# Optimization experiments

Hardware: AMD Instinct MI355X
Metric: run time of the kernel (lower is better)

The kernel has to match this reference:

```python
import jax, jax.numpy as jnp
import numpy as np

N_BLOCKS = 2
C = 64
N_HEADS = 4
FF = 256
NB_SEQ = 40
SEQ_LEN = 512
NB_PAIRS = (NB_SEQ * (NB_SEQ - 1)) // 2  # 780
B = 2
EPS_ATT = 1e-6


def _ln(x, g, b, eps=1e-5):
    # LayerNorm over last axis (channels)
    mu = jnp.mean(x, axis=-1, keepdims=True)
    var = jnp.var(x, axis=-1, keepdims=True)
    return (x - mu) * jax.lax.rsqrt(var + eps) * g + b


def _kernel_attn(x, wq, bq, wk, bk, wv, bv, wp, bp):
    # x: [B, M, T, C]; faithful to KernelAxialMultiAttention.
    Bs, M, T, Cc = x.shape
    N, D = N_HEADS, Cc // N_HEADS
    q = jax.nn.elu(x @ wq.T + bq) + 1.0
    k = jax.nn.elu(x @ wk.T + bk) + 1.0
    v = x @ wv.T + bv
    q = q.reshape(Bs, M, T, N, D)
    k = k.reshape(Bs, M, T, N, D)
    v = v.reshape(Bs, M, T, N, D)
    ksum = k.sum(axis=2)                                   # [B,M,N,D]
    z = 1.0 / (jnp.einsum('bmtnd,bmnd->bmtn', q, ksum) + EPS_ATT)  # [B,M,T,N]
    ktv = jnp.einsum('bmtnd,bmtne->bmnde', k, v)           # [B,M,N,D,D]
    # Original does Z.expand(...,T,D) @ KtV where Z's D columns are identical,
    # which equals z * column-sum of KtV (sum over first D axis).
    ktv_cs = ktv.sum(axis=-2)                              # [B,M,N,D]
    V = z[..., None] * ktv_cs[:, :, None, :, :]            # [B,M,T,N,D]
    V = V.reshape(Bs, M, T, Cc)
    return V @ wp.T + bp


def setup_inputs() -> dict:
    key = jax.random.key(0)
    ks = iter(jax.random.split(key, 64))

    def w(shape, scale=0.05):
        return jax.random.normal(next(ks), shape, dtype=jnp.float32) * scale

    # seq2pair gather matrix [P, S]
    ii, jj = np.triu_indices(NB_SEQ, 1)
    sp = np.zeros((NB_PAIRS, NB_SEQ), np.float32)
    sp[np.arange(NB_PAIRS), ii] = 1.0
    sp[np.arange(NB_PAIRS), jj] = 1.0

    inp = {
        'x': jax.random.normal(next(ks), (B, 22, SEQ_LEN, NB_SEQ), dtype=jnp.float32),
        'w_in': w((C, 22)), 'b_in': jnp.zeros((C,), jnp.float32),
        'g0': jnp.ones((C,), jnp.float32), 'be0': jnp.zeros((C,), jnp.float32),
        'rqw': w((N_BLOCKS, C, C)), 'rqb': jnp.zeros((N_BLOCKS, C), jnp.float32),
        'rkw': w((N_BLOCKS, C, C)), 'rkb': jnp.zeros((N_BLOCKS, C), jnp.float32),
        'rvw': w((N_BLOCKS, C, C)), 'rvb': jnp.zeros((N_BLOCKS, C), jnp.float32),
        'rpw': w((N_BLOCKS, C, C)), 'rpb': jnp.zeros((N_BLOCKS, C), jnp.float32),
        'cqw': w((N_BLOCKS, C, C)), 'cqb': jnp.zeros((N_BLOCKS, C), jnp.float32),
        'ckw': w((N_BLOCKS, C, C)), 'ckb': jnp.zeros((N_BLOCKS, C), jnp.float32),
        'cvw': w((N_BLOCKS, C, C)), 'cvb': jnp.zeros((N_BLOCKS, C), jnp.float32),
        'cpw': w((N_BLOCKS, C, C)), 'cpb': jnp.zeros((N_BLOCKS, C), jnp.float32),
        'ln_g': jnp.ones((N_BLOCKS, C), jnp.float32), 'ln_b': jnp.zeros((N_BLOCKS, C), jnp.float32),
        'f1w': w((N_BLOCKS, FF, C)), 'f1b': jnp.zeros((N_BLOCKS, FF), jnp.float32),
        'f2w': w((N_BLOCKS, C, FF)), 'f2b': jnp.zeros((N_BLOCKS, C), jnp.float32),
        'wout': w((1, C)), 'bout': jnp.zeros((1,), jnp.float32),
        'seq2pair': jnp.asarray(sp),
    }
    return inp


def reference(x, w_in, b_in, g0, be0, rqw, rqb, rkw, rkb, rvw, rvb, rpw, rpb,
              cqw, cqb, ckw, ckb, cvw, cvb, cpw, cpb, ln_g, ln_b,
              f1w, f1b, f2w, f2b, wout, bout, seq2pair):
    # block_1_1: 1x1 conv (22->64) + ReLU; x: [B,22,L,S] -> h: [B,C,L,S]
    h = jax.nn.relu(jnp.einsum('bcls,dc->bdls', x, w_in) + b_in[None, :, None, None])
    # seq2pair gather-sum: [B,P,L,C] channel-last representation
    hp = jnp.einsum('ps,bdls->bpld', seq2pair, h)
    hp = _ln(hp, g0, be0)
    for i in range(N_BLOCKS):
        # row attention over seq_len axis (M=P, T=L)
        att = _kernel_attn(hp, rqw[i], rqb[i], rkw[i], rkb[i], rvw[i], rvb[i], rpw[i], rpb[i])
        hp = att + hp
        hp = _ln(hp, ln_g[i], ln_b[i])
        # column attention over pairs axis (M=L, T=P)
        hc = jnp.swapaxes(hp, 1, 2)  # [B,L,P,C]
        att = _kernel_attn(hc, cqw[i], cqb[i], ckw[i], ckb[i], cvw[i], cvb[i], cpw[i], cpb[i])
        hp = jnp.swapaxes(att, 1, 2) + hp
        hp = _ln(hp, ln_g[i], ln_b[i])
        # FFN: 1x1 conv 64->256 GELU 256->64, residual
        f = jax.nn.gelu(hp @ f1w[i].T + f1b[i], approximate=False)
        hp = (f @ f2w[i].T + f2b[i]) + hp
        if i != N_BLOCKS - 1:
            hp = _ln(hp, ln_g[i], ln_b[i])
    # pwFNN: 1x1 conv 64->1 + Softplus, then mean over seq_len axis
    y = jax.nn.softplus(hp @ wout.T + bout)[..., 0]   # [B,P,L]
    return jnp.mean(y, axis=-1)                        # [B,P]
```

## Files before the change

### kernel.cpp

```cpp
#include <hip/hip_runtime.h>
#include <math.h>
#include <stdint.h>

#define B_   2
#define S_   40
#define P_   780
#define L_   512
#define C_   64
#define FF_  256
#define NTOK (B_*P_*L_)

typedef __attribute__((ext_vector_type(8))) short short8;
typedef __attribute__((ext_vector_type(4))) float f32x4;
typedef __attribute__((ext_vector_type(4))) unsigned int u32x4;

__device__ __forceinline__ float ln64(float r, float g, float b) {
    float s1 = r, s2 = r * r;
    #pragma unroll
    for (int m = 1; m < 64; m <<= 1) {
        s1 += __shfl_xor(s1, m, 64);
        s2 += __shfl_xor(s2, m, 64);
    }
    float mu  = s1 * (1.0f / 64.0f);
    float var = s2 * (1.0f / 64.0f) - mu * mu;
    return (r - mu) * rsqrtf(var + 1e-5f) * g + b;
}

__device__ __forceinline__ float gelu_fast(float x) {
    float x2 = x * x;
    float u  = x * fmaf(0.044715f, x2, 1.0f);
    float e  = __builtin_amdgcn_exp2f(u * 2.302265106f);
    return x * e * __builtin_amdgcn_rcpf(e + 1.0f);
}
__device__ __forceinline__ float softplus_f(float v) {
    return (v > 20.0f) ? v : log1pf(__expf(v));
}
__device__ __forceinline__ float elup1(float v) {
    return (v > 0.0f) ? v + 1.0f : __expf(v);
}
__device__ __forceinline__ unsigned short f2bf(float f) {
    union { float f; uint32_t u; } cv; cv.f = f;
    uint32_t u = cv.u;
    return (unsigned short)((u + 0x7FFFu + ((u >> 16) & 1u)) >> 16);
}
__device__ __forceinline__ short8 pack8(f32x4 a, f32x4 b) {
    short8 v;
    v[0]=(short)f2bf(a[0]); v[1]=(short)f2bf(a[1]); v[2]=(short)f2bf(a[2]); v[3]=(short)f2bf(a[3]);
    v[4]=(short)f2bf(b[0]); v[5]=(short)f2bf(b[1]); v[6]=(short)f2bf(b[2]); v[7]=(short)f2bf(b[3]);
    return v;
}
__device__ __forceinline__ uint32_t cvtpk(float a, float b) {
    uint32_t d;
    asm("v_cvt_pk_bf16_f32 %0, %1, %2" : "=v"(d) : "v"(a), "v"(b));
    return d;
}

__global__ void k_conv_in(const float* __restrict__ x, const float* __restrict__ w_in,
                          const float* __restrict__ b_in, float* __restrict__ h) {
    int gid = blockIdx.x * 256 + threadIdx.x;
    int c  = gid & 63;
    int tk = gid >> 6;
    if (tk >= B_ * L_ * S_) return;
    int b = tk / (L_ * S_);
    int r = tk % (L_ * S_);
    int l = r / S_;
    int s = r % S_;
    float acc = b_in[c];
    const float* xb = x + (size_t)b * 22 * L_ * S_ + (size_t)l * S_ + s;
    #pragma unroll
    for (int cc = 0; cc < 22; cc++)
        acc = fmaf(xb[(size_t)cc * L_ * S_], w_in[c * 22 + cc], acc);
    h[gid] = fmaxf(acc, 0.0f);
}

__global__ void k_gather_ln(const float* __restrict__ h, const float* __restrict__ g0,
                            const float* __restrict__ be0, float* __restrict__ hp) {
    int lane = threadIdx.x & 63;
    int wv   = threadIdx.x >> 6;
    int tk = blockIdx.x * 4 + wv;
    if (tk >= NTOK) return;
    int b = tk / (P_ * L_);
    int r = tk % (P_ * L_);
    int p = r / L_;
    int l = r % L_;
    int i = 0, rem = p, cnt = S_ - 1;
    while (rem >= cnt) { rem -= cnt; cnt--; i++; }
    int j = i + 1 + rem;
    const float* hb = h + (((size_t)b * L_ + l) * S_) * 64;
    float v = hb[i * 64 + lane] + hb[j * 64 + lane];
    hp[(size_t)tk * 64 + lane] = ln64(v, g0[lane], be0[lane]);
}

__global__ void k_wprep_qkv(const float* __restrict__ rqw, const float* __restrict__ rkw,
                            const float* __restrict__ rvw, const float* __restrict__ cqw,
                            const float* __restrict__ ckw, const float* __restrict__ cvw,
                            unsigned short* __restrict__ qkvf) {
    int g = blockIdx.x * 256 + threadIdx.x;
    if (g >= 6144) return;
    int m = g >> 9, r = g & 511;
    int mat = m >> 1, layer = m & 1;
    int q = r >> 6, lane = r & 63;
    int c = lane & 15, hi = lane >> 4;
    int nt = q >> 1, s = q & 1;
    const float* base;
    switch (mat) {
        case 0: base = rqw; break; case 1: base = rkw; break; case 2: base = rvw; break;
        case 3: base = cqw; break; case 4: base = ckw; break; default: base = cvw; break;
    }
    const float* src = base + layer * 4096 + (nt * 16 + c) * 64 + s * 32 + hi * 8;
    short8 v;
    #pragma unroll
    for (int i = 0; i < 8; i++) v[i] = (short)f2bf(src[i]);
    *(short8*)(qkvf + (size_t)m * 4096 + (size_t)r * 8) = v;
}

template <bool ROW>
__global__ __launch_bounds__(512) void k_attn_red(
        const float* __restrict__ hp, const unsigned short* __restrict__ wkf,
        const unsigned short* __restrict__ wvf, const float* __restrict__ bk,
        const float* __restrict__ bv, const float* __restrict__ wp,
        float* __restrict__ stats) {
    __shared__ float redK[8][64];
    __shared__ float redV[8][64];
    __shared__ float kvfin[64];

    const int tid = threadIdx.x, lane = tid & 63, w8 = tid >> 6;
    const int t = lane & 15, hi = lane >> 4;
    const int slice = blockIdx.x;
    const int T  = ROW ? L_ : P_;
    const int NT = ROW ? 32 : 49;

    size_t rowbase, rowstep;
    if (ROW) { rowbase = (size_t)slice * L_ * 64; rowstep = 64; }
    else     { int b = slice >> 9, l = slice & 511;
               rowbase = ((size_t)b * P_ * L_ + l) * 64; rowstep = (size_t)L_ * 64; }

    short8 wkfr[4][2], wvfr[4][2];
    #pragma unroll
    for (int nt = 0; nt < 4; nt++)
        #pragma unroll
        for (int s = 0; s < 2; s++) {
            wkfr[nt][s] = *(const short8*)(wkf + ((size_t)((nt*2+s)*64 + lane)) * 8);
            wvfr[nt][s] = *(const short8*)(wvf + ((size_t)((nt*2+s)*64 + lane)) * 8);
        }
    f32x4 bkL[4], bvL[4];
    #pragma unroll
    for (int nt = 0; nt < 4; nt++) {
        bkL[nt] = *(const f32x4*)(bk + nt * 16 + hi * 4);
        bvL[nt] = *(const f32x4*)(bv + nt * 16 + hi * 4);
    }

    float ks[4][4] = {}, kv[4][4] = {};

    for (int tile = w8; tile < NT; tile += 8) {
        int tok = tile * 16 + t;
        bool valid = ROW || (tok < T);
        int tokc = valid ? tok : (T - 1);
        const float* src = hp + rowbase + (size_t)tokc * rowstep;
        short8 xf[2];
        #pragma unroll
        for (int s = 0; s < 2; s++) {
            f32x4 a  = *(const f32x4*)(src + s * 32 + hi * 8);
            f32x4 b2 = *(const f32x4*)(src + s * 32 + hi * 8 + 4);
            xf[s] = pack8(a, b2);
        }
        f32x4 aK[4], aV[4];
        #pragma unroll
        for (int nt = 0; nt < 4; nt++) { aK[nt] = (f32x4){0,0,0,0}; aV[nt] = (f32x4){0,0,0,0}; }
        #pragma unroll
        for (int nt = 0; nt < 4; nt++)
            #pragma unroll
            for (int s = 0; s < 2; s++) {
                aK[nt] = __builtin_amdgcn_mfma_f32_16x16x32_bf16(wkfr[nt][s], xf[s], aK[nt], 0, 0, 0);
                aV[nt] = __builtin_amdgcn_mfma_f32_16x16x32_bf16(wvfr[nt][s], xf[s], aV[nt], 0, 0, 0);
            }
        #pragma unroll
        for (int nt = 0; nt < 4; nt++) {
            float kk[4], vv[4];
            #pragma unroll
            for (int r = 0; r < 4; r++) {
                kk[r] = valid ? elup1(aK[nt][r] + bkL[nt][r]) : 0.0f;
                vv[r] = valid ? (aV[nt][r] + bvL[nt][r]) : 0.0f;
            }
            float sp = kk[0] + kk[1] + kk[2] + kk[3];
            sp += __shfl_xor(sp, 16, 64);
            sp += __shfl_xor(sp, 32, 64);
            #pragma unroll
            for (int r = 0; r < 4; r++) { ks[nt][r] += kk[r]; kv[nt][r] += sp * vv[r]; }
        }
    }

    #pragma unroll
    for (int nt = 0; nt < 4; nt++)
        #pragma unroll
        for (int r = 0; r < 4; r++) {
            #pragma unroll
            for (int m = 1; m < 16; m <<= 1) {
                ks[nt][r] += __shfl_xor(ks[nt][r], m, 64);
                kv[nt][r] += __shfl_xor(kv[nt][r], m, 64);
            }
        }
    if (t == 0) {
        #pragma unroll
        for (int nt = 0; nt < 4; nt++)
            #pragma unroll
            for (int r = 0; r < 4; r++) {
                redK[w8][nt * 16 + hi * 4 + r] = ks[nt][r];
                redV[w8][nt * 16 + hi * 4 + r] = kv[nt][r];
            }
    }
    __syncthreads();
    if (tid < 64) {
        float a = 0.0f, b2 = 0.0f;
        #pragma unroll
        for (int w = 0; w < 8; w++) { a += redK[w][tid]; b2 += redV[w][tid]; }
        stats[(size_t)slice * 320 + tid] = a;
        kvfin[tid] = b2;
    }
    __syncthreads();
    if (tid < 256) {
        int c = tid & 63, n = tid >> 6;
        const float* wpr = wp + c * 64 + n * 16;
        float s = 0.0f;
        #pragma unroll
        for (int e = 0; e < 16; e++) s = fmaf(kvfin[n * 16 + e], wpr[e], s);
        stats[(size_t)slice * 320 + 64 + c * 4 + n] = s;
    }
}

__global__ __launch_bounds__(256) void k_attn_map_row(
        float* __restrict__ hp, const unsigned short* __restrict__ wqf,
        const float* __restrict__ bq, const float* __restrict__ bp,
        const float* __restrict__ stats, const float* __restrict__ lng,
        const float* __restrict__ lnb) {
    const int tid = threadIdx.x, lane = tid & 63, w4 = tid >> 6;
    const int t = lane & 15, hi = lane >> 4;
    const int slice = blockIdx.x >> 3;
    const int tok = ((blockIdx.x & 7) * 4 + w4) * 16 + t;
    const size_t off = ((size_t)slice * L_ + tok) * 64;

    const float* src = hp + off;
    short8 xf[2];
    #pragma unroll
    for (int s = 0; s < 2; s++) {
        f32x4 a  = *(const f32x4*)(src + s * 32 + hi * 8);
        f32x4 b2 = *(const f32x4*)(src + s * 32 + hi * 8 + 4);
        xf[s] = pack8(a, b2);
    }
    f32x4 aQ[4];
    #pragma unroll
    for (int nt = 0; nt < 4; nt++) aQ[nt] = (f32x4){0,0,0,0};
    #pragma unroll
    for (int nt = 0; nt < 4; nt++)
        #pragma unroll
        for (int s = 0; s < 2; s++) {
            short8 wfr = *(const short8*)(wqf + ((size_t)((nt*2+s)*64 + lane)) * 8);
            aQ[nt] = __builtin_amdgcn_mfma_f32_16x16x32_bf16(wfr, xf[s], aQ[nt], 0, 0, 0);
        }

    const float* st = stats + (size_t)slice * 320;
    float z[4];
    #pragma unroll
    for (int nt = 0; nt < 4; nt++) {
        f32x4 bq4 = *(const f32x4*)(bq + nt * 16 + hi * 4);
        f32x4 kS  = *(const f32x4*)(st + nt * 16 + hi * 4);
        float d = 0.0f;
        #pragma unroll
        for (int r = 0; r < 4; r++)
            d = fmaf(elup1(aQ[nt][r] + bq4[r]), kS[r], d);
        d += __shfl_xor(d, 16, 64);
        d += __shfl_xor(d, 32, 64);
        z[nt] = 1.0f / (d + 1e-6f);
    }

    float o[4][4];
    float s1 = 0.0f, s2 = 0.0f;
    #pragma unroll
    for (int nt = 0; nt < 4; nt++) {
        f32x4 bp4 = *(const f32x4*)(bp + nt * 16 + hi * 4);
        f32x4 xr  = *(const f32x4*)(src + nt * 16 + hi * 4);
        #pragma unroll
        for (int r = 0; r < 4; r++) {
            int ch = nt * 16 + hi * 4 + r;
            f32x4 wv4 = *(const f32x4*)(st + 64 + ch * 4);
            float val = z[0] * wv4[0] + z[1] * wv4[1] + z[2] * wv4[2] + z[3] * wv4[3]
                      + bp4[r] + xr[r];
            o[nt][r] = val;
            s1 += val; s2 += val * val;
        }
    }
    s1 += __shfl_xor(s1, 16, 64);  s1 += __shfl_xor(s1, 32, 64);
    s2 += __shfl_xor(s2, 16, 64);  s2 += __shfl_xor(s2, 32, 64);
    float mu  = s1 * (1.0f / 64.0f);
    float var = s2 * (1.0f / 64.0f) - mu * mu;
    float rs  = rsqrtf(var + 1e-5f);
    #pragma unroll
    for (int nt = 0; nt < 4; nt++) {
        f32x4 g4 = *(const f32x4*)(lng + nt * 16 + hi * 4);
        f32x4 b4 = *(const f32x4*)(lnb + nt * 16 + hi * 4);
        f32x4 res;
        #pragma unroll
        for (int r = 0; r < 4; r++)
            res[r] = (o[nt][r] - mu) * rs * g4[r] + b4[r];
        *(f32x4*)(hp + off + nt * 16 + hi * 4) = res;
    }
}

__global__ void k_wprep(const float* __restrict__ f1w, const float* __restrict__ f2w,
                        unsigned short* __restrict__ w1s, unsigned short* __restrict__ w2s) {
    int g = blockIdx.x * 256 + threadIdx.x;
    if (g >= 8192) return;
    int layer = g >> 12;
    int rem   = g & 4095;
    int which = rem >> 11;
    int idx   = rem & 2047;
    int l  = idx & 63;
    int q  = idx >> 6;
    int c  = l & 15, hi = l >> 4;
    const float* src;
    unsigned short* dst;
    if (which == 0) {
        int s = q & 1, nt = q >> 1;
        src = f1w + (size_t)layer * 16384 + (nt * 16 + c) * 64 + s * 32 + hi * 8;
        dst = w1s + (size_t)layer * 16384 + (size_t)idx * 8;
    } else {
        int s = q & 7, nt = q >> 3;
        src = f2w + (size_t)layer * 16384 + (nt * 16 + c) * 256 + s * 32 + hi * 8;
        dst = w2s + (size_t)layer * 16384 + (size_t)idx * 8;
    }
    short8 v;
    #pragma unroll
    for (int i = 0; i < 8; i++) v[i] = (short)f2bf(src[i]);
    *(short8*)dst = v;
}

template <int MODE>
__global__ __launch_bounds__(256) void k_cmap_ffn(
        float* __restrict__ hp, const unsigned short* __restrict__ wqf,
        const float* __restrict__ bq, const float* __restrict__ bpv,
        const float* __restrict__ stats,
        const unsigned short* __restrict__ w1s, const float* __restrict__ f1b,
        const unsigned short* __restrict__ w2s, const float* __restrict__ f2b,
        const float* __restrict__ lng, const float* __restrict__ lnb,
        const float* __restrict__ wout, const float* __restrict__ bout,
        float* __restrict__ out) {
    __shared__ __align__(16) unsigned char Ylds[4][2048];
    __shared__ __align__(16) unsigned char G2[4][8192];

    const int tid = threadIdx.x, lane = tid & 63, wv = tid >> 6;
    const int c = lane & 15, hi = lane >> 4;
    const int slice = blockIdx.x / 13, tile = blockIdx.x % 13;
    const int b = slice >> 9, l = slice & 511;
    const int p = (tile * 4 + wv) * 16 + c;
    const bool valid = p < P_;
    const int pc = valid ? p : P_ - 1;
    const size_t off = (((size_t)b * P_ + pc) * L_ + l) * 64;
    const float* src = hp + off;

    short8 xf[2];
    #pragma unroll
    for (int s = 0; s < 2; s++) {
        f32x4 a  = *(const f32x4*)(src + s * 32 + hi * 8);
        f32x4 b2 = *(const f32x4*)(src + s * 32 + hi * 8 + 4);
        xf[s] = pack8(a, b2);
    }
    f32x4 aQ[4];
    #pragma unroll
    for (int nt = 0; nt < 4; nt++) aQ[nt] = (f32x4){0,0,0,0};
    #pragma unroll
    for (int nt = 0; nt < 4; nt++)
        #pragma unroll
        for (int s = 0; s < 2; s++) {
            short8 wfr = *(const short8*)(wqf + ((size_t)((nt*2+s)*64 + lane)) * 8);
            aQ[nt] = __builtin_amdgcn_mfma_f32_16x16x32_bf16(wfr, xf[s], aQ[nt], 0, 0, 0);
        }
    const float* st = stats + (size_t)slice * 320;
    float z[4];
    #pragma unroll
    for (int nt = 0; nt < 4; nt++) {
        f32x4 bq4 = *(const f32x4*)(bq + nt * 16 + hi * 4);
        f32x4 kS  = *(const f32x4*)(st + nt * 16 + hi * 4);
        float d = 0.0f;
        #pragma unroll
        for (int r = 0; r < 4; r++)
            d = fmaf(elup1(aQ[nt][r] + bq4[r]), kS[r], d);
        d += __shfl_xor(d, 16, 64);
        d += __shfl_xor(d, 32, 64);
        z[nt] = 1.0f / (d + 1e-6f);
    }

    float vv[4][4];
    {
        float s1 = 0.0f, s2 = 0.0f;
        #pragma unroll
        for (int nt = 0; nt < 4; nt++) {
            f32x4 bp4 = *(const f32x4*)(bpv + nt * 16 + hi * 4);
            f32x4 xr  = *(const f32x4*)(src + nt * 16 + hi * 4);
            #pragma unroll
            for (int r = 0; r < 4; r++) {
                int ch = nt * 16 + hi * 4 + r;
                f32x4 wv4 = *(const f32x4*)(st + 64 + ch * 4);
                float val = z[0] * wv4[0] + z[1] * wv4[1] + z[2] * wv4[2] + z[3] * wv4[3]
                          + bp4[r] + xr[r];
                vv[nt][r] = val;
                s1 += val; s2 += val * val;
            }
        }
        s1 += __shfl_xor(s1, 16, 64);  s1 += __shfl_xor(s1, 32, 64);
        s2 += __shfl_xor(s2, 16, 64);  s2 += __shfl_xor(s2, 32, 64);
        float mu  = s1 * (1.0f / 64.0f);
        float var = s2 * (1.0f / 64.0f) - mu * mu;
        float rs  = rsqrtf(var + 1e-5f);
        #pragma unroll
        for (int nt = 0; nt < 4; nt++) {
            f32x4 g4 = *(const f32x4*)(lng + nt * 16 + hi * 4);
            f32x4 b4 = *(const f32x4*)(lnb + nt * 16 + hi * 4);
            #pragma unroll
            for (int r = 0; r < 4; r++)
                vv[nt][r] = (vv[nt][r] - mu) * rs * g4[r] + b4[r];
        }
    }

    unsigned char* yw = &Ylds[wv][0];
    #pragma unroll
    for (int nt = 0; nt < 4; nt++) {
        uint2 w = make_uint2(cvtpk(vv[nt][0], vv[nt][1]), cvtpk(vv[nt][2], vv[nt][3]));
        uint32_t ch0 = nt * 16 + hi * 4;
        uint32_t boff = (uint32_t)c * 128 + ((ch0 >> 3) ^ (uint32_t)(c & 7)) * 16 + (ch0 & 7) * 2;
        *(uint2*)(yw + boff) = w;
    }
    short8 xb2[2];
    #pragma unroll
    for (int s = 0; s < 2; s++)
        xb2[s] = *(short8*)(yw + (uint32_t)c * 128 +
                            (((uint32_t)(s * 4 + hi)) ^ (uint32_t)(c & 7)) * 16);

    unsigned char* g2w = &G2[wv][0] + c * 512;
    #pragma unroll
    for (int nt = 0; nt < 16; nt++) {
        f32x4 acc = *(const f32x4*)(f1b + nt * 16 + hi * 4);
        #pragma unroll
        for (int s = 0; s < 2; s++) {
            short8 wf = *(const short8*)(w1s + ((size_t)(nt * 2 + s) * 64 + lane) * 8);
            acc = __builtin_amdgcn_mfma_f32_16x16x32_bf16(wf, xb2[s], acc, 0, 0, 0);
        }
        uint32_t p0 = cvtpk(gelu_fast(acc[0]), gelu_fast(acc[1]));
        uint32_t p1 = cvtpk(gelu_fast(acc[2]), gelu_fast(acc[3]));
        uint32_t woff = ((uint32_t)(nt * 32 + hi * 8)) ^ ((uint32_t)c << 4);
        *(uint2*)(g2w + woff) = make_uint2(p0, p1);
    }

    f32x4 acc2[4];
    #pragma unroll
    for (int n2 = 0; n2 < 4; n2++)
        acc2[n2] = *(const f32x4*)(f2b + n2 * 16 + hi * 4);
    #pragma unroll
    for (int s = 0; s < 8; s++) {
        uint32_t roff = ((uint32_t)(s * 64 + hi * 16)) ^ ((uint32_t)c << 4);
        short8 fa = *(short8*)(g2w + roff);
        #pragma unroll
        for (int n2 = 0; n2 < 4; n2++) {
            short8 wf = *(const short8*)(w2s + ((size_t)(n2 * 8 + s) * 64 + lane) * 8);
            acc2[n2] = __builtin_amdgcn_mfma_f32_16x16x32_bf16(wf, fa, acc2[n2], 0, 0, 0);
        }
    }

    float vo[4][4];
    float s1 = 0.0f, s2 = 0.0f;
    #pragma unroll
    for (int n2 = 0; n2 < 4; n2++)
        #pragma unroll
        for (int r = 0; r < 4; r++) {
            float v = acc2[n2][r] + vv[n2][r];
            vo[n2][r] = v;
            s1 += v; s2 += v * v;
        }

    if (MODE == 0) {
        s1 += __shfl_xor(s1, 16, 64);  s1 += __shfl_xor(s1, 32, 64);
        s2 += __shfl_xor(s2, 16, 64);  s2 += __shfl_xor(s2, 32, 64);
        float mu  = s1 * (1.0f / 64.0f);
        float var = s2 * (1.0f / 64.0f) - mu * mu;
        float rs  = rsqrtf(var + 1e-5f);
        if (valid) {
            float* drow = hp + off;
            #pragma unroll
            for (int n2 = 0; n2 < 4; n2++) {
                f32x4 g4 = *(const f32x4*)(lng + n2 * 16 + hi * 4);
                f32x4 b4 = *(const f32x4*)(lnb + n2 * 16 + hi * 4);
                f32x4 res;
                #pragma unroll
                for (int r = 0; r < 4; r++)
                    res[r] = (vo[n2][r] - mu) * rs * g4[r] + b4[r];
                *(f32x4*)(drow + n2 * 16 + hi * 4) = res;
            }
        }
    } else {
        float part = 0.0f;
        #pragma unroll
        for (int n2 = 0; n2 < 4; n2++) {
            f32x4 w4 = *(const f32x4*)(wout + n2 * 16 + hi * 4);
            #pragma unroll
            for (int r = 0; r < 4; r++)
                part = fmaf(vo[n2][r], w4[r], part);
        }
        part += __shfl_xor(part, 16, 64);
        part += __shfl_xor(part, 32, 64);
        if (hi == 0 && valid) {
            float sp = softplus_f(part + bout[0]);
            atomicAdd(out + b * P_ + pc, sp * (1.0f / L_));
        }
    }
}

extern "C" void kernel_launch(void* const* d_in, const int* in_sizes, int n_in,
                              void* d_out, int out_size, void* d_ws, size_t ws_size,
                              hipStream_t stream) {
    const float* x    = (const float*)d_in[0];
    const float* w_in = (const float*)d_in[1];
    const float* b_in = (const float*)d_in[2];
    const float* g0   = (const float*)d_in[3];
    const float* be0  = (const float*)d_in[4];
    const float* rqw  = (const float*)d_in[5];  const float* rqb = (const float*)d_in[6];
    const float* rkw  = (const float*)d_in[7];  const float* rkb = (const float*)d_in[8];
    const float* rvw  = (const float*)d_in[9];  const float* rvb = (const float*)d_in[10];
    const float* rpw  = (const float*)d_in[11]; const float* rpb = (const float*)d_in[12];
    const float* cqw  = (const float*)d_in[13]; const float* cqb = (const float*)d_in[14];
    const float* ckw  = (const float*)d_in[15]; const float* ckb = (const float*)d_in[16];
    const float* cvw  = (const float*)d_in[17]; const float* cvb = (const float*)d_in[18];
    const float* cpw  = (const float*)d_in[19]; const float* cpb = (const float*)d_in[20];
    const float* lng  = (const float*)d_in[21]; const float* lnb = (const float*)d_in[22];
    const float* f1w  = (const float*)d_in[23]; const float* f1b = (const float*)d_in[24];
    const float* f2w  = (const float*)d_in[25]; const float* f2b = (const float*)d_in[26];
    const float* wout = (const float*)d_in[27]; const float* bout= (const float*)d_in[28];
    float* out = (float*)d_out;

    float* hp = (float*)d_ws;
    float* h  = hp + (size_t)NTOK * 64;
    unsigned short* w1s  = (unsigned short*)h;
    unsigned short* w2s  = w1s + 2 * 16384;
    unsigned short* qkvf = w2s + 2 * 16384;
    float* stats = (float*)(qkvf + 12 * 4096);

    hipMemsetAsync(out, 0, (size_t)out_size * sizeof(float), stream);

    k_conv_in<<<(B_ * L_ * S_ * 64) / 256, 256, 0, stream>>>(x, w_in, b_in, h);
    k_gather_ln<<<NTOK / 4, 256, 0, stream>>>(h, g0, be0, hp);
    k_wprep<<<32, 256, 0, stream>>>(f1w, f2w, w1s, w2s);
    k_wprep_qkv<<<24, 256, 0, stream>>>(rqw, rkw, rvw, cqw, ckw, cvw, qkvf);

    for (int i = 0; i < 2; i++) {
        k_attn_red<true><<<B_ * P_, 512, 0, stream>>>(hp,
            qkvf + (size_t)(2 + i) * 4096, qkvf + (size_t)(4 + i) * 4096,
            rkb + i * 64, rvb + i * 64, rpw + i * 4096, stats);
        k_attn_map_row<<<B_ * P_ * 8, 256, 0, stream>>>(hp,
            qkvf + (size_t)(0 + i) * 4096, rqb + i * 64, rpb + i * 64,
            stats, lng + i * 64, lnb + i * 64);
        k_attn_red<false><<<B_ * L_, 512, 0, stream>>>(hp,
            qkvf + (size_t)(8 + i) * 4096, qkvf + (size_t)(10 + i) * 4096,
            ckb + i * 64, cvb + i * 64, cpw + i * 4096, stats);
        if (i == 0) {
            k_cmap_ffn<0><<<B_ * L_ * 13, 256, 0, stream>>>(hp,
                qkvf + (size_t)(6 + i) * 4096, cqb + i * 64, cpb + i * 64, stats,
                w1s + (size_t)i * 16384, f1b + i * 256,
                w2s + (size_t)i * 16384, f2b + i * 64,
                lng + i * 64, lnb + i * 64, wout, bout, out);
        } else {
            k_cmap_ffn<1><<<B_ * L_ * 13, 256, 0, stream>>>(hp,
                qkvf + (size_t)(6 + i) * 4096, cqb + i * 64, cpb + i * 64, stats,
                w1s + (size_t)i * 16384, f1b + i * 256,
                w2s + (size_t)i * 16384, f2b + i * 64,
                lng + i * 64, lnb + i * 64, wout, bout, out);
        }
    }
}
```

Measured before the change: 1.171 ms.

## Store activations as bf16 with transposed copy for column attention

The activation buffer moves from fp32 to bf16 storage. The row-attention map kernel now writes a second, transposed [B,L,P,C] copy, so column-attention kernels read contiguous rows instead of doing strided gathers. The FFN GELU staging in LDS is split into two halves, which halves shared memory per block and may raise occupancy. This cuts global traffic and conversion work, but the residual stream now loses precision on every stage because it is rounded to bf16.

New measurement: 1.175 ms. Within noise of the previous version (+0.3%).

```diff
diff --git a/kernel.cpp b/kernel.cpp
--- a/kernel.cpp
+++ b/kernel.cpp
@@ -12,7 +12,7 @@
 
 typedef __attribute__((ext_vector_type(8))) short short8;
 typedef __attribute__((ext_vector_type(4))) float f32x4;
-typedef __attribute__((ext_vector_type(4))) unsigned int u32x4;
+typedef __attribute__((ext_vector_type(4))) unsigned short us4;
 
 __device__ __forceinline__ float ln64(float r, float g, float b) {
     float s1 = r, s2 = r * r;
@@ -25,7 +25,6 @@
     float var = s2 * (1.0f / 64.0f) - mu * mu;
     return (r - mu) * rsqrtf(var + 1e-5f) * g + b;
 }
-
 __device__ __forceinline__ float gelu_fast(float x) {
     float x2 = x * x;
     float u  = x * fmaf(0.044715f, x2, 1.0f);
@@ -43,11 +42,8 @@
     uint32_t u = cv.u;
     return (unsigned short)((u + 0x7FFFu + ((u >> 16) & 1u)) >> 16);
 }
-__device__ __forceinline__ short8 pack8(f32x4 a, f32x4 b) {
-    short8 v;
-    v[0]=(short)f2bf(a[0]); v[1]=(short)f2bf(a[1]); v[2]=(short)f2bf(a[2]); v[3]=(short)f2bf(a[3]);
-    v[4]=(short)f2bf(b[0]); v[5]=(short)f2bf(b[1]); v[6]=(short)f2bf(b[2]); v[7]=(short)f2bf(b[3]);
-    return v;
+__device__ __forceinline__ float bf2f(unsigned short u) {
+    union { uint32_t u; float f; } cv; cv.u = (uint32_t)u << 16; return cv.f;
 }
 __device__ __forceinline__ uint32_t cvtpk(float a, float b) {
     uint32_t d;
@@ -74,7 +70,7 @@
 }
 
 __global__ void k_gather_ln(const float* __restrict__ h, const float* __restrict__ g0,
-                            const float* __restrict__ be0, float* __restrict__ hp) {
+                            const float* __restrict__ be0, unsigned short* __restrict__ hp) {
     int lane = threadIdx.x & 63;
     int wv   = threadIdx.x >> 6;
     int tk = blockIdx.x * 4 + wv;
@@ -88,7 +84,7 @@
     int j = i + 1 + rem;
     const float* hb = h + (((size_t)b * L_ + l) * S_) * 64;
     float v = hb[i * 64 + lane] + hb[j * 64 + lane];
-    hp[(size_t)tk * 64 + lane] = ln64(v, g0[lane], be0[lane]);
+    hp[(size_t)tk * 64 + lane] = f2bf(ln64(v, g0[lane], be0[lane]));
 }
 
 __global__ void k_wprep_qkv(const float* __restrict__ rqw, const float* __restrict__ rkw,
@@ -116,7 +112,7 @@
 
 template <bool ROW>
 __global__ __launch_bounds__(512) void k_attn_red(
-        const float* __restrict__ hp, const unsigned short* __restrict__ wkf,
+        const unsigned short* __restrict__ xb, const unsigned short* __restrict__ wkf,
         const unsigned short* __restrict__ wvf, const float* __restrict__ bk,
         const float* __restrict__ bv, const float* __restrict__ wp,
         float* __restrict__ stats) {
@@ -129,11 +125,7 @@
     const int slice = blockIdx.x;
     const int T  = ROW ? L_ : P_;
     const int NT = ROW ? 32 : 49;
-
-    size_t rowbase, rowstep;
-    if (ROW) { rowbase = (size_t)slice * L_ * 64; rowstep = 64; }
-    else     { int b = slice >> 9, l = slice & 511;
-               rowbase = ((size_t)b * P_ * L_ + l) * 64; rowstep = (size_t)L_ * 64; }
+    const size_t base = (size_t)slice * (size_t)T * 64;
 
     short8 wkfr[4][2], wvfr[4][2];
     #pragma unroll
@@ -156,14 +148,11 @@
         int tok = tile * 16 + t;
         bool valid = ROW || (tok < T);
         int tokc = valid ? tok : (T - 1);
-        const float* src = hp + rowbase + (size_t)tokc * rowstep;
+        const unsigned short* src = xb + base + (size_t)tokc * 64;
         short8 xf[2];
         #pragma unroll
-        for (int s = 0; s < 2; s++) {
-            f32x4 a  = *(const f32x4*)(src + s * 32 + hi * 8);
-            f32x4 b2 = *(const f32x4*)(src + s * 32 + hi * 8 + 4);
-            xf[s] = pack8(a, b2);
-        }
+        for (int s = 0; s < 2; s++)
+            xf[s] = *(const short8*)(src + s * 32 + hi * 8);
         f32x4 aK[4], aV[4];
         #pragma unroll
         for (int nt = 0; nt < 4; nt++) { aK[nt] = (f32x4){0,0,0,0}; aV[nt] = (f32x4){0,0,0,0}; }
@@ -229,7 +218,8 @@
 }
 
 __global__ __launch_bounds__(256) void k_attn_map_row(
-        float* __restrict__ hp, const unsigned short* __restrict__ wqf,
+        const unsigned short* __restrict__ hp, unsigned short* __restrict__ hpT,
+        const unsigned short* __restrict__ wqf,
         const float* __restrict__ bq, const float* __restrict__ bp,
         const float* __restrict__ stats, const float* __restrict__ lng,
         const float* __restrict__ lnb) {
@@ -237,16 +227,13 @@
     const int t = lane & 15, hi = lane >> 4;
     const int slice = blockIdx.x >> 3;
     const int tok = ((blockIdx.x & 7) * 4 + w4) * 16 + t;
-    const size_t off = ((size_t)slice * L_ + tok) * 64;
-
-    const float* src = hp + off;
+    const unsigned short* src = hp + ((size_t)slice * L_ + tok) * 64;
+
     short8 xf[2];
     #pragma unroll
-    for (int s = 0; s < 2; s++) {
-        f32x4 a  = *(const f32x4*)(src + s * 32 + hi * 8);
-        f32x4 b2 = *(const f32x4*)(src + s * 32 + hi * 8 + 4);
-        xf[s] = pack8(a, b2);
-    }
+    for (int s = 0; s < 2; s++)
+        xf[s] = *(const short8*)(src + s * 32 + hi * 8);
+
     f32x4 aQ[4];
     #pragma unroll
     for (int nt = 0; nt < 4; nt++) aQ[nt] = (f32x4){0,0,0,0};
@@ -278,13 +265,13 @@
     #pragma unroll
     for (int nt = 0; nt < 4; nt++) {
         f32x4 bp4 = *(const f32x4*)(bp + nt * 16 + hi * 4);
-        f32x4 xr  = *(const f32x4*)(src + nt * 16 + hi * 4);
+        us4 xr4 = *(const us4*)(src + nt * 16 + hi * 4);
         #pragma unroll
         for (int r = 0; r < 4; r++) {
             int ch = nt * 16 + hi * 4 + r;
             f32x4 wv4 = *(const f32x4*)(st + 64 + ch * 4);
             float val = z[0] * wv4[0] + z[1] * wv4[1] + z[2] * wv4[2] + z[3] * wv4[3]
-                      + bp4[r] + xr[r];
+                      + bp4[r] + bf2f(xr4[r]);
             o[nt][r] = val;
             s1 += val; s2 += val * val;
         }
@@ -294,15 +281,18 @@
     float mu  = s1 * (1.0f / 64.0f);
     float var = s2 * (1.0f / 64.0f) - mu * mu;
     float rs  = rsqrtf(var + 1e-5f);
+
+    const int b = slice / P_, p = slice - b * P_;
+    unsigned short* dst = hpT + (((size_t)b * L_ + tok) * P_ + p) * 64;
     #pragma unroll
     for (int nt = 0; nt < 4; nt++) {
         f32x4 g4 = *(const f32x4*)(lng + nt * 16 + hi * 4);
         f32x4 b4 = *(const f32x4*)(lnb + nt * 16 + hi * 4);
-        f32x4 res;
-        #pragma unroll
-        for (int r = 0; r < 4; r++)
-            res[r] = (o[nt][r] - mu) * rs * g4[r] + b4[r];
-        *(f32x4*)(hp + off + nt * 16 + hi * 4) = res;
+        float r0 = (o[nt][0] - mu) * rs * g4[0] + b4[0];
+        float r1 = (o[nt][1] - mu) * rs * g4[1] + b4[1];
+        float r2 = (o[nt][2] - mu) * rs * g4[2] + b4[2];
+        float r3 = (o[nt][3] - mu) * rs * g4[3] + b4[3];
+        *(uint2*)(dst + nt * 16 + hi * 4) = make_uint2(cvtpk(r0, r1), cvtpk(r2, r3));
     }
 }
 
@@ -336,7 +326,8 @@
 
 template <int MODE>
 __global__ __launch_bounds__(256) void k_cmap_ffn(
-        float* __restrict__ hp, const unsigned short* __restrict__ wqf,
+        const unsigned short* __restrict__ hpT, unsigned short* __restrict__ hp,
+        const unsigned short* __restrict__ wqf,
         const float* __restrict__ bq, const float* __restrict__ bpv,
         const float* __restrict__ stats,
         const unsigned short* __restrict__ w1s, const float* __restrict__ f1b,
@@ -345,7 +336,7 @@
         const float* __restrict__ wout, const float* __restrict__ bout,
         float* __restrict__ out) {
     __shared__ __align__(16) unsigned char Ylds[4][2048];
-    __shared__ __align__(16) unsigned char G2[4][8192];
+    __shared__ __align__(16) unsigned char G2[4][4096];
 
     const int tid = threadIdx.x, lane = tid & 63, wv = tid >> 6;
     const int c = lane & 15, hi = lane >> 4;
@@ -354,16 +345,12 @@
     const int p = (tile * 4 + wv) * 16 + c;
     const bool valid = p < P_;
     const int pc = valid ? p : P_ - 1;
-    const size_t off = (((size_t)b * P_ + pc) * L_ + l) * 64;
-    const float* src = hp + off;
+    const unsigned short* src = hpT + ((size_t)slice * P_ + pc) * 64;
 
     short8 xf[2];
     #pragma unroll
-    for (int s = 0; s < 2; s++) {
-        f32x4 a  = *(const f32x4*)(src + s * 32 + hi * 8);
-        f32x4 b2 = *(const f32x4*)(src + s * 32 + hi * 8 + 4);
-        xf[s] = pack8(a, b2);
-    }
+    for (int s = 0; s < 2; s++)
+        xf[s] = *(const short8*)(src + s * 32 + hi * 8);
     f32x4 aQ[4];
     #pragma unroll
     for (int nt = 0; nt < 4; nt++) aQ[nt] = (f32x4){0,0,0,0};
@@ -395,13 +382,13 @@
         #pragma unroll
         for (int nt = 0; nt < 4; nt++) {
             f32x4 bp4 = *(const f32x4*)(bpv + nt * 16 + hi * 4);
-            f32x4 xr  = *(const f32x4*)(src + nt * 16 + hi * 4);
+            us4 xr4 = *(const us4*)(src + nt * 16 + hi * 4);
             #pragma unroll
             for (int r = 0; r < 4; r++) {
                 int ch = nt * 16 + hi * 4 + r;
                 f32x4 wv4 = *(const f32x4*)(st + 64 + ch * 4);
                 float val = z[0] * wv4[0] + z[1] * wv4[1] + z[2] * wv4[2] + z[3] * wv4[3]
-                          + bp4[r] + xr[r];
+                          + bp4[r] + bf2f(xr4[r]);
                 vv[nt][r] = val;
                 s1 += val; s2 += val * val;
             }
@@ -435,33 +422,38 @@
         xb2[s] = *(short8*)(yw + (uint32_t)c * 128 +
                             (((uint32_t)(s * 4 + hi)) ^ (uint32_t)(c & 7)) * 16);
 
-    unsigned char* g2w = &G2[wv][0] + c * 512;
-    #pragma unroll
-    for (int nt = 0; nt < 16; nt++) {
-        f32x4 acc = *(const f32x4*)(f1b + nt * 16 + hi * 4);
-        #pragma unroll
-        for (int s = 0; s < 2; s++) {
-            short8 wf = *(const short8*)(w1s + ((size_t)(nt * 2 + s) * 64 + lane) * 8);
-            acc = __builtin_amdgcn_mfma_f32_16x16x32_bf16(wf, xb2[s], acc, 0, 0, 0);
-        }
-        uint32_t p0 = cvtpk(gelu_fast(acc[0]), gelu_fast(acc[1]));
-        uint32_t p1 = cvtpk(gelu_fast(acc[2]), gelu_fast(acc[3]));
-        uint32_t woff = ((uint32_t)(nt * 32 + hi * 8)) ^ ((uint32_t)c << 4);
-        *(uint2*)(g2w + woff) = make_uint2(p0, p1);
-    }
-
     f32x4 acc2[4];
     #pragma unroll
     for (int n2 = 0; n2 < 4; n2++)
         acc2[n2] = *(const f32x4*)(f2b + n2 * 16 + hi * 4);
-    #pragma unroll
-    for (int s = 0; s < 8; s++) {
-        uint32_t roff = ((uint32_t)(s * 64 + hi * 16)) ^ ((uint32_t)c << 4);
-        short8 fa = *(short8*)(g2w + roff);
-        #pragma unroll
-        for (int n2 = 0; n2 < 4; n2++) {
-            short8 wf = *(const short8*)(w2s + ((size_t)(n2 * 8 + s) * 64 + lane) * 8);
-            acc2[n2] = __builtin_amdgcn_mfma_f32_16x16x32_bf16(wf, fa, acc2[n2], 0, 0, 0);
+
+    unsigned char* g2w = &G2[wv][0] + c * 256;
+    #pragma unroll
+    for (int half = 0; half < 2; half++) {
+        #pragma unroll
+        for (int ntl = 0; ntl < 8; ntl++) {
+            int nt = half * 8 + ntl;
+            f32x4 acc = *(const f32x4*)(f1b + nt * 16 + hi * 4);
+            #pragma unroll
+            for (int s = 0; s < 2; s++) {
+                short8 wf = *(const short8*)(w1s + ((size_t)(nt * 2 + s) * 64 + lane) * 8);
+                acc = __builtin_amdgcn_mfma_f32_16x16x32_bf16(wf, xb2[s], acc, 0, 0, 0);
+            }
+            uint32_t p0 = cvtpk(gelu_fast(acc[0]), gelu_fast(acc[1]));
+            uint32_t p1 = cvtpk(gelu_fast(acc[2]), gelu_fast(acc[3]));
+            uint32_t woff = ((uint32_t)(ntl * 32 + hi * 8)) ^ ((uint32_t)(c & 7) << 4);
+            *(uint2*)(g2w + woff) = make_uint2(p0, p1);
+        }
+        #pragma unroll
+        for (int sl = 0; sl < 4; sl++) {
+            int s = half * 4 + sl;
+            uint32_t roff = ((uint32_t)(sl * 64 + hi * 16)) ^ ((uint32_t)(c & 7) << 4);
+            short8 fa = *(short8*)(g2w + roff);
+            #pragma unroll
+            for (int n2 = 0; n2 < 4; n2++) {
+                short8 wf = *(const short8*)(w2s + ((size_t)(n2 * 8 + s) * 64 + lane) * 8);
+                acc2[n2] = __builtin_amdgcn_mfma_f32_16x16x32_bf16(wf, fa, acc2[n2], 0, 0, 0);
+            }
         }
     }
 
@@ -483,16 +475,16 @@
         float var = s2 * (1.0f / 64.0f) - mu * mu;
         float rs  = rsqrtf(var + 1e-5f);
         if (valid) {
-            float* drow = hp + off;
+            unsigned short* dst = hp + (((size_t)b * P_ + pc) * L_ + l) * 64;
             #pragma unroll
             for (int n2 = 0; n2 < 4; n2++) {
                 f32x4 g4 = *(const f32x4*)(lng + n2 * 16 + hi * 4);
                 f32x4 b4 = *(const f32x4*)(lnb + n2 * 16 + hi * 4);
-                f32x4 res;
-                #pragma unroll
-                for (int r = 0; r < 4; r++)
-                    res[r] = (vo[n2][r] - mu) * rs * g4[r] + b4[r];
-                *(f32x4*)(drow + n2 * 16 + hi * 4) = res;
+                float r0 = (vo[n2][0] - mu) * rs * g4[0] + b4[0];
+                float r1 = (vo[n2][1] - mu) * rs * g4[1] + b4[1];
+                float r2 = (vo[n2][2] - mu) * rs * g4[2] + b4[2];
+                float r3 = (vo[n2][3] - mu) * rs * g4[3] + b4[3];
+                *(uint2*)(dst + n2 * 16 + hi * 4) = make_uint2(cvtpk(r0, r1), cvtpk(r2, r3));
             }
         }
     } else {
@@ -535,8 +527,9 @@
     const float* wout = (const float*)d_in[27]; const float* bout= (const float*)d_in[28];
     float* out = (float*)d_out;
 
-    float* hp = (float*)d_ws;
-    float* h  = hp + (size_t)NTOK * 64;
+    unsigned short* hp  = (unsigned short*)d_ws;
+    unsigned short* hpT = hp + (size_t)NTOK * 64;
+    float* h = (float*)(hpT + (size_t)NTOK * 64);
     unsigned short* w1s  = (unsigned short*)h;
     unsigned short* w2s  = w1s + 2 * 16384;
     unsigned short* qkvf = w2s + 2 * 16384;
@@ -553,20 +546,20 @@
         k_attn_red<true><<<B_ * P_, 512, 0, stream>>>(hp,
             qkvf + (size_t)(2 + i) * 4096, qkvf + (size_t)(4 + i) * 4096,
             rkb + i * 64, rvb + i * 64, rpw + i * 4096, stats);
-        k_attn_map_row<<<B_ * P_ * 8, 256, 0, stream>>>(hp,
+        k_attn_map_row<<<B_ * P_ * 8, 256, 0, stream>>>(hp, hpT,
             qkvf + (size_t)(0 + i) * 4096, rqb + i * 64, rpb + i * 64,
             stats, lng + i * 64, lnb + i * 64);
-        k_attn_red<false><<<B_ * L_, 512, 0, stream>>>(hp,
+        k_attn_red<false><<<B_ * L_, 512, 0, stream>>>(hpT,
             qkvf + (size_t)(8 + i) * 4096, qkvf + (size_t)(10 + i) * 4096,
             ckb + i * 64, cvb + i * 64, cpw + i * 4096, stats);
         if (i == 0) {
-            k_cmap_ffn<0><<<B_ * L_ * 13, 256, 0, stream>>>(hp,
+            k_cmap_ffn<0><<<B_ * L_ * 13, 256, 0, stream>>>(hpT, hp,
                 qkvf + (size_t)(6 + i) * 4096, cqb + i * 64, cpb + i * 64, stats,
                 w1s + (size_t)i * 16384, f1b + i * 256,
                 w2s + (size_t)i * 16384, f2b + i * 64,
                 lng + i * 64, lnb + i * 64, wout, bout, out);
         } else {
-            k_cmap_ffn<1><<<B_ * L_ * 13, 256, 0, stream>>>(hp,
+            k_cmap_ffn<1><<<B_ * L_ * 13, 256, 0, stream>>>(hpT, hp,
                 qkvf + (size_t)(6 + i) * 4096, cqb + i * 64, cpb + i * 64, stats,
                 w1s + (size_t)i * 16384, f1b + i * 256,
                 w2s + (size_t)i * 16384, f2b + i * 64,
```
